# Kernel optimization log

Hardware: AMD Instinct MI355X
Metric: run time of the kernel (lower is better)

## Reference

```python
import jax, jax.numpy as jnp
import numpy as np

N = 50000   # nodes
E = 500000  # edges
G = 64      # graphs in batch
H = 2       # attention heads
D = 64      # hidden per head (hid)
F_IN = 4    # num_features
C = 5       # num_classes
NEG_SLOPE = 0.2


def setup_inputs() -> dict:
    key = jax.random.key(0)
    ks = jax.random.split(key, 24)
    inp = {
        'x': jax.random.normal(ks[0], (N, F_IN), jnp.float32),
        'edge_index': jax.random.randint(ks[1], (2, E), 0, N, dtype=jnp.int64),
        'batch': jnp.sort(jax.random.randint(ks[2], (N,), 0, G, dtype=jnp.int64)),
    }
    ins = [F_IN, H * D, H * D, H * D]
    ki = 3
    for l, fin in enumerate(ins, 1):
        s = 1.0 / np.sqrt(fin)
        inp[f'W{l}'] = s * jax.random.normal(ks[ki], (fin, H * D), jnp.float32); ki += 1
        inp[f'asrc{l}'] = 0.1 * jax.random.normal(ks[ki], (H, D), jnp.float32); ki += 1
        inp[f'adst{l}'] = 0.1 * jax.random.normal(ks[ki], (H, D), jnp.float32); ki += 1
        inp[f'b{l}'] = 0.01 * jax.random.normal(ks[ki], (H * D,), jnp.float32); ki += 1
    inp['lin_w'] = (1.0 / np.sqrt(H * D)) * jax.random.normal(ks[ki], (H * D, C), jnp.float32); ki += 1
    inp['lin_b'] = jnp.zeros((C,), jnp.float32)
    return inp


def gat_conv(x, src, dst, W, a_src, a_dst, b):
    # x: [N, Fin] -> h: [N, H, D]
    h = (x @ W).reshape(-1, H, D)
    alpha_src = jnp.sum(h * a_src, axis=-1)  # [N, H]
    alpha_dst = jnp.sum(h * a_dst, axis=-1)  # [N, H]
    e = jax.nn.leaky_relu(alpha_src[src] + alpha_dst[dst], NEG_SLOPE)  # [E, H]
    # segment softmax over incoming edges of each dst node
    e_max = jax.ops.segment_max(e, dst, num_segments=N)  # [N, H]
    e_exp = jnp.exp(e - e_max[dst])
    denom = jax.ops.segment_sum(e_exp, dst, num_segments=N)
    alpha = e_exp / (denom[dst] + 1e-16)  # [E, H]
    msg = h[src] * alpha[:, :, None]  # [E, H, D]
    out = jax.ops.segment_sum(msg, dst, num_segments=N)  # [N, H, D]
    return out.reshape(-1, H * D) + b


def reference(x, edge_index, batch,
              W1, asrc1, adst1, b1,
              W2, asrc2, adst2, b2,
              W3, asrc3, adst3, b3,
              W4, asrc4, adst4, b4,
              lin_w, lin_b):
    src, dst = edge_index[0], edge_index[1]
    h = jax.nn.relu(gat_conv(x, src, dst, W1, asrc1, adst1, b1))
    h = jax.nn.relu(gat_conv(h, src, dst, W2, asrc2, adst2, b2))
    h = jax.nn.relu(gat_conv(h, src, dst, W3, asrc3, adst3, b3))
    h = jax.nn.relu(gat_conv(h, src, dst, W4, asrc4, adst4, b4))
    # global mean pool over graphs
    sums = jax.ops.segment_sum(h, batch, num_segments=G)  # [G, 128]
    counts = jax.ops.segment_sum(jnp.ones((h.shape[0],), h.dtype), batch, num_segments=G)
    pooled = sums / jnp.maximum(counts, 1.0)[:, None]
    return jax.nn.sigmoid(pooled @ lin_w + lin_b)  # [G, C]
```

## Files before the change

kernel.cpp:

```cpp
#include <hip/hip_runtime.h>
#include <math.h>

#define NHEAD 2
#define NDIM  64
#define HD    128
#define NGRAPH 64
#define NCLS  5
#define NEG_SLOPE 0.2f
#define LDA 136

typedef __attribute__((ext_vector_type(8))) short bf16x8;
typedef __attribute__((ext_vector_type(4))) float f32x4;

static __device__ __forceinline__ unsigned short f2bf(float f) {
    unsigned int u = __float_as_uint(f);
    u = (u + 0x7fff + ((u >> 16) & 1)) >> 16;
    return (unsigned short)u;
}
static __device__ __forceinline__ float bf2f(unsigned short b) {
    return __uint_as_float((unsigned int)b << 16);
}


__global__ void k_deg(const int* __restrict__ dst, int* __restrict__ deg, int E) {
    int i = blockIdx.x * blockDim.x + threadIdx.x;
    if (i < E) atomicAdd(&deg[dst[i]], 1);
}

__global__ __launch_bounds__(256) void k_scan_local(const int* __restrict__ deg,
                                                    int* __restrict__ ptr,
                                                    int* __restrict__ bsum, int n) {
    __shared__ int wsum[4];
    const int tid = threadIdx.x, lane = tid & 63, wid = tid >> 6;
    const int base = blockIdx.x * 2048 + tid * 8;
    int v[8];
    #pragma unroll
    for (int k = 0; k < 8; ++k) {
        int i = base + k;
        v[k] = (i < n) ? deg[i] : 0;
    }
    #pragma unroll
    for (int k = 1; k < 8; ++k) v[k] += v[k - 1];
    int x = v[7];
    #pragma unroll
    for (int off = 1; off < 64; off <<= 1) {
        int t = __shfl_up(x, off, 64);
        if (lane >= off) x += t;
    }
    if (lane == 63) wsum[wid] = x;
    __syncthreads();
    int woff = 0;
    #pragma unroll
    for (int k = 0; k < 4; ++k) woff += (k < wid) ? wsum[k] : 0;
    int texcl = woff + x - v[7];
    #pragma unroll
    for (int k = 0; k < 8; ++k) {
        int i = base + k;
        if (i < n) ptr[i + 1] = texcl + v[k];
    }
    if (tid == 255) bsum[blockIdx.x] = woff + x;
    if (blockIdx.x == 0 && tid == 0) ptr[0] = 0;
}

__global__ void k_scan_bsum(int* __restrict__ bsum, int B) {
    int lane = threadIdx.x;
    int carry = 0;
    for (int base = 0; base < B; base += 64) {
        int i = base + lane;
        int v = (i < B) ? bsum[i] : 0;
        int x = v;
        #pragma unroll
        for (int off = 1; off < 64; off <<= 1) {
            int t = __shfl_up(x, off, 64);
            if (lane >= off) x += t;
        }
        if (i < B) bsum[i] = carry + x - v;
        carry += __shfl(x, 63, 64);
    }
}

__global__ __launch_bounds__(256) void k_scan_add(int* __restrict__ ptr,
                                                  const int* __restrict__ bsum, int n) {
    int off = bsum[blockIdx.x];
    if (off == 0) return;
    const int base = blockIdx.x * 2048 + threadIdx.x * 8;
    #pragma unroll
    for (int k = 0; k < 8; ++k) {
        int i = base + k;
        if (i < n) ptr[i + 1] += off;
    }
}

__global__ void k_scatter(const int* __restrict__ src, const int* __restrict__ dst,
                          const int* __restrict__ ptr, int* __restrict__ fill,
                          int* __restrict__ csr, int E) {
    int i = blockIdx.x * blockDim.x + threadIdx.x;
    if (i < E) {
        int d = dst[i];
        int pos = atomicAdd(&fill[d], 1);
        csr[ptr[d] + pos] = src[i];
    }
}


__global__ void k_prepw(const float* __restrict__ W2, const float* __restrict__ W3,
                        const float* __restrict__ W4, unsigned short* __restrict__ Wt) {
    int idx = blockIdx.x * blockDim.x + threadIdx.x;
    if (idx >= 3 * HD * HD) return;
    int l = idx / (HD * HD), rem = idx % (HD * HD);
    int n = rem >> 7, k = rem & 127;
    const float* W = (l == 0) ? W2 : (l == 1) ? W3 : W4;
    Wt[idx] = f2bf(W[k * HD + n]);
}

__global__ void k_gemm1_alpha(const float* __restrict__ x, const float* __restrict__ W,
                              const float* __restrict__ asrc, const float* __restrict__ adst,
                              unsigned short* __restrict__ out, float* __restrict__ oas,
                              float* __restrict__ oad, int N) {
    int n = (blockIdx.x * blockDim.x + threadIdx.x) >> 6;
    int lane = threadIdx.x & 63;
    if (n >= N) return;
    float4 xv = *(const float4*)&x[n * 4];
    int c0 = lane * 2;
    float2 w0 = *(const float2*)&W[c0];
    float2 w1 = *(const float2*)&W[128 + c0];
    float2 w2 = *(const float2*)&W[256 + c0];
    float2 w3 = *(const float2*)&W[384 + c0];
    float v0 = xv.x * w0.x + xv.y * w1.x + xv.z * w2.x + xv.w * w3.x;
    float v1 = xv.x * w0.y + xv.y * w1.y + xv.z * w2.y + xv.w * w3.y;
    unsigned short b0 = f2bf(v0), b1 = f2bf(v1);
    unsigned int packed = (unsigned int)b0 | ((unsigned int)b1 << 16);
    *(unsigned int*)&out[(size_t)n * HD + c0] = packed;
    float vx = bf2f(b0), vy = bf2f(b1);
    float2 av = *(const float2*)&asrc[c0];
    float2 dv = *(const float2*)&adst[c0];
    float s = vx * av.x + vy * av.y;
    float t = vx * dv.x + vy * dv.y;
    #pragma unroll
    for (int off = 16; off > 0; off >>= 1) {
        s += __shfl_xor(s, off);
        t += __shfl_xor(t, off);
    }
    if ((lane & 31) == 0) {
        int head = lane >> 5;
        oas[n * 2 + head] = s;
        oad[n * 2 + head] = t;
    }
}

static __device__ __forceinline__ uint4 agg_row(
    const unsigned short* __restrict__ h, const float* __restrict__ oas,
    const float* __restrict__ oad, const int* __restrict__ ptr,
    const int* __restrict__ csr, const float* __restrict__ bias,
    int n, int N, int sub, int gbase, int hsel) {
    const bool valid = (n < N);
    int beg = 0, end = 0;
    float2 adn = make_float2(0.f, 0.f);
    if (valid) {
        beg = ptr[n]; end = ptr[n + 1];
        adn = *(const float2*)&oad[n * 2];
    }
    float m0 = -INFINITY, m1 = -INFINITY, l0 = 0.f, l1 = 0.f;
    float acc[8];
    #pragma unroll
    for (int k = 0; k < 8; ++k) acc[k] = 0.f;

    auto accum = [&](uint4 hv, float pj) {
        #pragma unroll
        for (int k = 0; k < 4; ++k) {
            unsigned int u = (&hv.x)[k];
            acc[2 * k]     += pj * __uint_as_float(u << 16);
            acc[2 * k + 1] += pj * __uint_as_float(u & 0xffff0000u);
        }
    };

    int cbeg = beg;
    while (__any(cbeg < end)) {
        int rem = end - cbeg;
        int cnt = rem < 0 ? 0 : (rem > 16 ? 16 : rem);
        int s = 0;
        float e0 = -INFINITY, e1 = -INFINITY;
        if (sub < cnt) {
            s = csr[cbeg + sub];
            float2 as = *(const float2*)&oas[s * 2];
            e0 = as.x + adn.x; e0 = (e0 >= 0.f) ? e0 : NEG_SLOPE * e0;
            e1 = as.y + adn.y; e1 = (e1 >= 0.f) ? e1 : NEG_SLOPE * e1;
        }
        float c0 = e0, c1 = e1;
        #pragma unroll
        for (int off = 8; off > 0; off >>= 1) {
            c0 = fmaxf(c0, __shfl_xor(c0, off));
            c1 = fmaxf(c1, __shfl_xor(c1, off));
        }
        float nm0 = fmaxf(m0, c0), nm1 = fmaxf(m1, c1);
        float sc0 = (nm0 == -INFINITY) ? 0.f : __expf(m0 - nm0);
        float sc1 = (nm1 == -INFINITY) ? 0.f : __expf(m1 - nm1);
        float p0 = (sub < cnt) ? __expf(e0 - nm0) : 0.f;
        float p1 = (sub < cnt) ? __expf(e1 - nm1) : 0.f;
        float s0 = p0, s1 = p1;
        #pragma unroll
        for (int off = 8; off > 0; off >>= 1) {
            s0 += __shfl_xor(s0, off);
            s1 += __shfl_xor(s1, off);
        }
        l0 = l0 * sc0 + s0;
        l1 = l1 * sc1 + s1;
        m0 = nm0; m1 = nm1;
        float scl = hsel ? sc1 : sc0;
        #pragma unroll
        for (int k = 0; k < 8; ++k) acc[k] *= scl;

        int jm = cnt;
        jm = max(jm, __shfl_xor(jm, 16));
        jm = max(jm, __shfl_xor(jm, 32));

        auto fetchp = [&](int j, uint4& hv, float& pj) {
            int sj = __shfl(s, gbase + j);
            float pa = __shfl(p0, gbase + j);
            float pb = __shfl(p1, gbase + j);
            pj = hsel ? pb : pa;
            hv = make_uint4(0, 0, 0, 0);
            if (j < cnt)
                hv = *(const uint4*)&h[(size_t)sj * HD + sub * 8];
        };
        uint4 hA, hB = make_uint4(0, 0, 0, 0);
        float pA, pB = 0.f;
        fetchp(0, hA, pA);
        if (jm > 1) fetchp(1, hB, pB);
        for (int j = 2; j < jm; ++j) {
            uint4 hC; float pC;
            fetchp(j, hC, pC);
            accum(hA, pA);
            hA = hB; pA = pB;
            hB = hC; pB = pC;
        }
        accum(hA, pA);
        if (jm > 1) accum(hB, pB);

        cbeg += 16;
    }

    uint4 pk = make_uint4(0, 0, 0, 0);
    if (valid) {
        float lsel = hsel ? l1 : l0;
        float inv = 1.f / (lsel + 1e-16f);
        float4 ba = *(const float4*)&bias[sub * 8];
        float4 bb = *(const float4*)&bias[sub * 8 + 4];
        float o[8];
        o[0] = fmaxf(acc[0] * inv + ba.x, 0.f);
        o[1] = fmaxf(acc[1] * inv + ba.y, 0.f);
        o[2] = fmaxf(acc[2] * inv + ba.z, 0.f);
        o[3] = fmaxf(acc[3] * inv + ba.w, 0.f);
        o[4] = fmaxf(acc[4] * inv + bb.x, 0.f);
        o[5] = fmaxf(acc[5] * inv + bb.y, 0.f);
        o[6] = fmaxf(acc[6] * inv + bb.z, 0.f);
        o[7] = fmaxf(acc[7] * inv + bb.w, 0.f);
        pk.x = (unsigned int)f2bf(o[0]) | ((unsigned int)f2bf(o[1]) << 16);
        pk.y = (unsigned int)f2bf(o[2]) | ((unsigned int)f2bf(o[3]) << 16);
        pk.z = (unsigned int)f2bf(o[4]) | ((unsigned int)f2bf(o[5]) << 16);
        pk.w = (unsigned int)f2bf(o[6]) | ((unsigned int)f2bf(o[7]) << 16);
    }
    return pk;
}

__global__ __launch_bounds__(256, 8) void k_agg_gemm(
    const unsigned short* __restrict__ hin,
    const float* __restrict__ oas_in, const float* __restrict__ oad_in,
    const int* __restrict__ ptr, const int* __restrict__ csr,
    const float* __restrict__ bias,
    const unsigned short* __restrict__ Wt,
    const float* __restrict__ asrc, const float* __restrict__ adst,
    unsigned short* __restrict__ hout,
    float* __restrict__ oas_out, float* __restrict__ oad_out, int N) {
    __shared__ unsigned short As[16 * LDA];
    __shared__ float psL[4][16], pdL[4][16];
    const int tid = threadIdx.x;
    const int lane = tid & 63, w = tid >> 6;
    const int grp = lane >> 4, sub = lane & 15;
    const int gbase = lane & 48;
    const int hsel = sub >> 3;
    const int nbase = blockIdx.x * 16;

    const int row = w * 4 + grp;
    uint4 pk = agg_row(hin, oas_in, oad_in, ptr, csr, bias,
                       nbase + row, N, sub, gbase, hsel);
    *(uint4*)&As[(size_t)row * LDA + sub * 8] = pk;
    __syncthreads();

    float av2[2], dv2[2];
    #pragma unroll
    for (int i = 0; i < 2; ++i) {
        int c = w * 2 + i;
        av2[i] = asrc[c * 16 + sub];
        dv2[i] = adst[c * 16 + sub];
    }
    f32x4 acc[2];
    acc[0] = (f32x4)(0.f);
    acc[1] = (f32x4)(0.f);
    #pragma unroll
    for (int ks = 0; ks < 4; ++ks) {
        bf16x8 a0 = *(const bf16x8*)&As[(size_t)sub * LDA + ks * 32 + grp * 8];
        #pragma unroll
        for (int i = 0; i < 2; ++i) {
            int c = w * 2 + i;
            bf16x8 b = *(const bf16x8*)&Wt[(size_t)(c * 16 + sub) * HD + ks * 32 + grp * 8];
            acc[i] = __builtin_amdgcn_mfma_f32_16x16x32_bf16(a0, b, acc[i], 0, 0, 0);
        }
    }

    const int rowb = nbase + grp * 4;
    #pragma unroll
    for (int i = 0; i < 2; ++i) {
        int col = (w * 2 + i) * 16 + sub;
        #pragma unroll
        for (int r = 0; r < 4; ++r) {
            int rw = rowb + r;
            if (rw < N) hout[(size_t)rw * HD + col] = f2bf(acc[i][r]);
        }
    }
    #pragma unroll
    for (int r = 0; r < 4; ++r) {
        float ps = acc[0][r] * av2[0] + acc[1][r] * av2[1];
        float pd = acc[0][r] * dv2[0] + acc[1][r] * dv2[1];
        #pragma unroll
        for (int off = 1; off < 16; off <<= 1) {
            ps += __shfl_xor(ps, off);
            pd += __shfl_xor(pd, off);
        }
        if (sub == 0) {
            psL[w][grp * 4 + r] = ps;
            pdL[w][grp * 4 + r] = pd;
        }
    }
    __syncthreads();
    if (tid < 32) {
        int r2 = tid & 15, head = tid >> 4;
        int n2 = nbase + r2;
        if (n2 < N) {
            float s = psL[2 * head][r2] + psL[2 * head + 1][r2];
            float d = pdL[2 * head][r2] + pdL[2 * head + 1][r2];
            oas_out[n2 * 2 + head] = s;
            oad_out[n2 * 2 + head] = d;
        }
    }
}

__global__ __launch_bounds__(256) void k_agg_final(
    const unsigned short* __restrict__ hin,
    const float* __restrict__ oas_in, const float* __restrict__ oad_in,
    const int* __restrict__ ptr, const int* __restrict__ csr,
    const float* __restrict__ bias,
    unsigned short* __restrict__ out, int N) {
    const int tid = threadIdx.x;
    const int lane = tid & 63;
    const int grp = lane >> 4, sub = lane & 15;
    const int gbase = lane & 48;
    const int hsel = sub >> 3;
    const int n = ((blockIdx.x * blockDim.x + tid) >> 6) * 4 + grp;
    uint4 pk = agg_row(hin, oas_in, oad_in, ptr, csr, bias, n, N, sub, gbase, hsel);
    if (n < N) *(uint4*)&out[(size_t)n * HD + sub * 8] = pk;
}

__global__ void k_pool(const unsigned short* __restrict__ feat, const int* __restrict__ batch,
                       float* __restrict__ pooled, int* __restrict__ gcount, int N) {
    int col = threadIdx.x;
    int n0 = blockIdx.x * 128;
    int n1 = min(n0 + 128, N);
    float acc = 0.f;
    int curg = -1, runlen = 0;
    for (int n = n0; n < n1; ++n) {
        int g = batch[n];
        if (g != curg) {
            if (curg >= 0) {
                atomicAdd(&pooled[curg * HD + col], acc);
                if (col == 0) atomicAdd(&gcount[curg], runlen);
            }
            acc = 0.f; runlen = 0;
            curg = g;
        }
        acc += bf2f(feat[(size_t)n * HD + col]);
        runlen++;
    }
    if (curg >= 0) {
        atomicAdd(&pooled[curg * HD + col], acc);
        if (col == 0) atomicAdd(&gcount[curg], runlen);
    }
}

__global__ void k_final(const float* __restrict__ pooled, const int* __restrict__ gcount,
                        const float* __restrict__ lw, const float* __restrict__ lb,
                        float* __restrict__ out) {
    int tid = threadIdx.x;
    if (tid >= NGRAPH * NCLS) return;
    int g = tid / NCLS, c = tid % NCLS;
    float cnt = fmaxf((float)gcount[g], 1.f);
    const float* p = pooled + g * HD;
    float sum = 0.f;
    for (int k = 0; k < HD; ++k)
        sum += p[k] * lw[k * NCLS + c];
    float z = lb[c] + sum / cnt;
    out[tid] = 1.f / (1.f + __expf(-z));
}


static inline size_t al256(size_t x) { return (x + 255) & ~(size_t)255; }

extern "C" void kernel_launch(void* const* d_in, const int* in_sizes, int n_in,
                              void* d_out, int out_size, void* d_ws, size_t ws_size,
                              hipStream_t stream) {
    const int N = in_sizes[0] / 4;
    const int E = in_sizes[1] / 2;

    const float* x     = (const float*)d_in[0];
    const int*   esrc  = (const int*)d_in[1];
    const int*   edst  = esrc + E;
    const int*   batch = (const int*)d_in[2];
    const float* Wl[4]  = {(const float*)d_in[3],  (const float*)d_in[7],
                           (const float*)d_in[11], (const float*)d_in[15]};
    const float* asr[4] = {(const float*)d_in[4],  (const float*)d_in[8],
                           (const float*)d_in[12], (const float*)d_in[16]};
    const float* ads[4] = {(const float*)d_in[5],  (const float*)d_in[9],
                           (const float*)d_in[13], (const float*)d_in[17]};
    const float* bs[4]  = {(const float*)d_in[6],  (const float*)d_in[10],
                           (const float*)d_in[14], (const float*)d_in[18]};
    const float* lin_w = (const float*)d_in[19];
    const float* lin_b = (const float*)d_in[20];
    float* out = (float*)d_out;

    char* w = (char*)d_ws;
    size_t off = 0;
    auto alloc = [&](size_t bytes) -> void* {
        void* p = w + off;
        off = al256(off + bytes);
        return p;
    };
    int*   deg    = (int*)alloc((size_t)N * 4);
    int*   fill   = (int*)alloc((size_t)N * 4);
    int*   gcount = (int*)alloc((size_t)NGRAPH * 4);
    float* pooled = (float*)alloc((size_t)NGRAPH * HD * 4);
    size_t zbytes = off;
    int*   ptr    = (int*)alloc((size_t)(N + 1) * 4);
    int*   bsum   = (int*)alloc((size_t)1024 * 4);
    int*   csr    = (int*)alloc((size_t)E * 4);
    unsigned short* hA   = (unsigned short*)alloc((size_t)N * HD * 2);
    unsigned short* hB   = (unsigned short*)alloc((size_t)N * HD * 2);
    unsigned short* feat = (unsigned short*)alloc((size_t)N * HD * 2);
    unsigned short* Wt   = (unsigned short*)alloc((size_t)3 * HD * HD * 2);
    float* asA = (float*)alloc((size_t)N * 2 * 4);
    float* adA = (float*)alloc((size_t)N * 2 * 4);
    float* asB = (float*)alloc((size_t)N * 2 * 4);
    float* adB = (float*)alloc((size_t)N * 2 * 4);
    (void)ws_size; (void)n_in; (void)out_size;

    hipMemsetAsync(d_ws, 0, zbytes, stream);

    k_prepw<<<(3 * HD * HD + 255) / 256, 256, 0, stream>>>(Wl[1], Wl[2], Wl[3], Wt);
    k_deg<<<(E + 255) / 256, 256, 0, stream>>>(edst, deg, E);
    const int SB = (N + 2047) / 2048;
    k_scan_local<<<SB, 256, 0, stream>>>(deg, ptr, bsum, N);
    k_scan_bsum<<<1, 64, 0, stream>>>(bsum, SB);
    k_scan_add<<<SB, 256, 0, stream>>>(ptr, bsum, N);
    k_scatter<<<(E + 255) / 256, 256, 0, stream>>>(esrc, edst, ptr, fill, csr, E);

    const int fused_blocks = (N + 15) / 16;

    k_gemm1_alpha<<<(N + 3) / 4, 256, 0, stream>>>(
        x, Wl[0], asr[0], ads[0], hA, asA, adA, N);
    k_agg_gemm<<<fused_blocks, 256, 0, stream>>>(
        hA, asA, adA, ptr, csr, bs[0], Wt,
        asr[1], ads[1], hB, asB, adB, N);
    k_agg_gemm<<<fused_blocks, 256, 0, stream>>>(
        hB, asB, adB, ptr, csr, bs[1], Wt + (size_t)HD * HD,
        asr[2], ads[2], hA, asA, adA, N);
    k_agg_gemm<<<fused_blocks, 256, 0, stream>>>(
        hA, asA, adA, ptr, csr, bs[2], Wt + (size_t)2 * HD * HD,
        asr[3], ads[3], hB, asB, adB, N);
    k_agg_final<<<(N + 15) / 16, 256, 0, stream>>>(
        hB, asB, adB, ptr, csr, bs[3], feat, N);

    k_pool<<<(N + 127) / 128, 128, 0, stream>>>(feat, batch, pooled, gcount, N);
    k_final<<<1, 320, 0, stream>>>(pooled, gcount, lin_w, lin_b, out);
}
```

Before: 371.4 us.

## Precompute softmax denominators per node and drop online max in aggregation

Adds a pre-pass kernel per layer that computes each destination node's softmax denominator without max subtraction, clamping logits at 80 to avoid overflow. The aggregation then computes each edge weight directly as exp(e)*inv, with each lane walking the edges and issuing four gathers at a time, replacing the online-softmax rescaling, shuffles and cross-lane max and sum reductions. The fused GEMM output is also staged through shared memory so each row is written with coalesced 16-byte stores. The cost is an extra kernel launch and a second pass over the CSR edges per layer, plus a possible precision change from skipping max subtraction.

After: 357.5 us. -3.7%, faster.

```diff
diff --git a/kernel.cpp b/kernel.cpp
--- a/kernel.cpp
+++ b/kernel.cpp
@@ -148,124 +148,105 @@
     }
 }
 
-static __device__ __forceinline__ uint4 agg_row(
+__global__ __launch_bounds__(256) void k_node_inv(const int* __restrict__ ptr,
+                                                  const int* __restrict__ csr,
+                                                  const float* __restrict__ oas,
+                                                  const float* __restrict__ oad,
+                                                  float* __restrict__ invL, int N) {
+    int t = blockIdx.x * blockDim.x + threadIdx.x;
+    int n = t >> 2, l4 = t & 3;
+    if (n >= N) return;
+    int beg = ptr[n], end = ptr[n + 1];
+    float2 ad2 = *(const float2*)&oad[n * 2];
+    float s0 = 0.f, s1 = 0.f;
+    for (int j = beg + l4; j < end; j += 4) {
+        int s = csr[j];
+        float2 as2 = *(const float2*)&oas[s * 2];
+        float e0 = as2.x + ad2.x; e0 = (e0 >= 0.f) ? e0 : NEG_SLOPE * e0;
+        float e1 = as2.y + ad2.y; e1 = (e1 >= 0.f) ? e1 : NEG_SLOPE * e1;
+        e0 = fminf(e0, 80.f); e1 = fminf(e1, 80.f);
+        s0 += __expf(e0); s1 += __expf(e1);
+    }
+    s0 += __shfl_xor(s0, 1); s0 += __shfl_xor(s0, 2);
+    s1 += __shfl_xor(s1, 1); s1 += __shfl_xor(s1, 2);
+    if (l4 == 0)
+        *(float2*)&invL[n * 2] = make_float2(1.f / (s0 + 1e-16f), 1.f / (s1 + 1e-16f));
+}
+
+static __device__ __forceinline__ void agg_acc(
     const unsigned short* __restrict__ h, const float* __restrict__ oas,
-    const float* __restrict__ oad, const int* __restrict__ ptr,
-    const int* __restrict__ csr, const float* __restrict__ bias,
-    int n, int N, int sub, int gbase, int hsel) {
-    const bool valid = (n < N);
-    int beg = 0, end = 0;
-    float2 adn = make_float2(0.f, 0.f);
-    if (valid) {
-        beg = ptr[n]; end = ptr[n + 1];
-        adn = *(const float2*)&oad[n * 2];
-    }
-    float m0 = -INFINITY, m1 = -INFINITY, l0 = 0.f, l1 = 0.f;
-    float acc[8];
+    const float* __restrict__ oad, const float* __restrict__ invL,
+    const int* __restrict__ ptr, const int* __restrict__ csr,
+    int n, int N, int sub, int hsel, float* acc) {
     #pragma unroll
     for (int k = 0; k < 8; ++k) acc[k] = 0.f;
-
-    auto accum = [&](uint4 hv, float pj) {
+    if (n >= N) return;
+    const int beg = ptr[n], end = ptr[n + 1];
+    const float adh = oad[n * 2 + hsel];
+    const float inv = invL[n * 2 + hsel];
+
+    auto alpha = [&](float as) {
+        float e = as + adh;
+        e = (e >= 0.f) ? e : NEG_SLOPE * e;
+        e = fminf(e, 80.f);
+        return __expf(e) * inv;
+    };
+    auto accum = [&](uint4 hv, float a) {
         #pragma unroll
         for (int k = 0; k < 4; ++k) {
             unsigned int u = (&hv.x)[k];
-            acc[2 * k]     += pj * __uint_as_float(u << 16);
-            acc[2 * k + 1] += pj * __uint_as_float(u & 0xffff0000u);
+            acc[2 * k]     += a * __uint_as_float(u << 16);
+            acc[2 * k + 1] += a * __uint_as_float(u & 0xffff0000u);
         }
     };
 
-    int cbeg = beg;
-    while (__any(cbeg < end)) {
-        int rem = end - cbeg;
-        int cnt = rem < 0 ? 0 : (rem > 16 ? 16 : rem);
-        int s = 0;
-        float e0 = -INFINITY, e1 = -INFINITY;
-        if (sub < cnt) {
-            s = csr[cbeg + sub];
-            float2 as = *(const float2*)&oas[s * 2];
-            e0 = as.x + adn.x; e0 = (e0 >= 0.f) ? e0 : NEG_SLOPE * e0;
-            e1 = as.y + adn.y; e1 = (e1 >= 0.f) ? e1 : NEG_SLOPE * e1;
-        }
-        float c0 = e0, c1 = e1;
-        #pragma unroll
-        for (int off = 8; off > 0; off >>= 1) {
-            c0 = fmaxf(c0, __shfl_xor(c0, off));
-            c1 = fmaxf(c1, __shfl_xor(c1, off));
-        }
-        float nm0 = fmaxf(m0, c0), nm1 = fmaxf(m1, c1);
-        float sc0 = (nm0 == -INFINITY) ? 0.f : __expf(m0 - nm0);
-        float sc1 = (nm1 == -INFINITY) ? 0.f : __expf(m1 - nm1);
-        float p0 = (sub < cnt) ? __expf(e0 - nm0) : 0.f;
-        float p1 = (sub < cnt) ? __expf(e1 - nm1) : 0.f;
-        float s0 = p0, s1 = p1;
-        #pragma unroll
-        for (int off = 8; off > 0; off >>= 1) {
-            s0 += __shfl_xor(s0, off);
-            s1 += __shfl_xor(s1, off);
-        }
-        l0 = l0 * sc0 + s0;
-        l1 = l1 * sc1 + s1;
-        m0 = nm0; m1 = nm1;
-        float scl = hsel ? sc1 : sc0;
-        #pragma unroll
-        for (int k = 0; k < 8; ++k) acc[k] *= scl;
-
-        int jm = cnt;
-        jm = max(jm, __shfl_xor(jm, 16));
-        jm = max(jm, __shfl_xor(jm, 32));
-
-        auto fetchp = [&](int j, uint4& hv, float& pj) {
-            int sj = __shfl(s, gbase + j);
-            float pa = __shfl(p0, gbase + j);
-            float pb = __shfl(p1, gbase + j);
-            pj = hsel ? pb : pa;
-            hv = make_uint4(0, 0, 0, 0);
-            if (j < cnt)
-                hv = *(const uint4*)&h[(size_t)sj * HD + sub * 8];
-        };
-        uint4 hA, hB = make_uint4(0, 0, 0, 0);
-        float pA, pB = 0.f;
-        fetchp(0, hA, pA);
-        if (jm > 1) fetchp(1, hB, pB);
-        for (int j = 2; j < jm; ++j) {
-            uint4 hC; float pC;
-            fetchp(j, hC, pC);
-            accum(hA, pA);
-            hA = hB; pA = pB;
-            hB = hC; pB = pC;
-        }
-        accum(hA, pA);
-        if (jm > 1) accum(hB, pB);
-
-        cbeg += 16;
-    }
-
-    uint4 pk = make_uint4(0, 0, 0, 0);
-    if (valid) {
-        float lsel = hsel ? l1 : l0;
-        float inv = 1.f / (lsel + 1e-16f);
-        float4 ba = *(const float4*)&bias[sub * 8];
-        float4 bb = *(const float4*)&bias[sub * 8 + 4];
-        float o[8];
-        o[0] = fmaxf(acc[0] * inv + ba.x, 0.f);
-        o[1] = fmaxf(acc[1] * inv + ba.y, 0.f);
-        o[2] = fmaxf(acc[2] * inv + ba.z, 0.f);
-        o[3] = fmaxf(acc[3] * inv + ba.w, 0.f);
-        o[4] = fmaxf(acc[4] * inv + bb.x, 0.f);
-        o[5] = fmaxf(acc[5] * inv + bb.y, 0.f);
-        o[6] = fmaxf(acc[6] * inv + bb.z, 0.f);
-        o[7] = fmaxf(acc[7] * inv + bb.w, 0.f);
-        pk.x = (unsigned int)f2bf(o[0]) | ((unsigned int)f2bf(o[1]) << 16);
-        pk.y = (unsigned int)f2bf(o[2]) | ((unsigned int)f2bf(o[3]) << 16);
-        pk.z = (unsigned int)f2bf(o[4]) | ((unsigned int)f2bf(o[5]) << 16);
-        pk.w = (unsigned int)f2bf(o[6]) | ((unsigned int)f2bf(o[7]) << 16);
-    }
+    int j = beg;
+    for (; j + 4 <= end; j += 4) {
+        int s0 = csr[j], s1 = csr[j + 1], s2 = csr[j + 2], s3 = csr[j + 3];
+        uint4 h0 = *(const uint4*)&h[(size_t)s0 * HD + sub * 8];
+        uint4 h1 = *(const uint4*)&h[(size_t)s1 * HD + sub * 8];
+        uint4 h2 = *(const uint4*)&h[(size_t)s2 * HD + sub * 8];
+        uint4 h3 = *(const uint4*)&h[(size_t)s3 * HD + sub * 8];
+        float x0 = oas[s0 * 2 + hsel], x1 = oas[s1 * 2 + hsel];
+        float x2 = oas[s2 * 2 + hsel], x3 = oas[s3 * 2 + hsel];
+        accum(h0, alpha(x0));
+        accum(h1, alpha(x1));
+        accum(h2, alpha(x2));
+        accum(h3, alpha(x3));
+    }
+    for (; j < end; ++j) {
+        int s = csr[j];
+        uint4 hv = *(const uint4*)&h[(size_t)s * HD + sub * 8];
+        float xs = oas[s * 2 + hsel];
+        accum(hv, alpha(xs));
+    }
+}
+
+static __device__ __forceinline__ uint4 bias_relu_pack(
+    const float* acc, const float* __restrict__ bias, int sub) {
+    float4 ba = *(const float4*)&bias[sub * 8];
+    float4 bb = *(const float4*)&bias[sub * 8 + 4];
+    float o[8];
+    o[0] = fmaxf(acc[0] + ba.x, 0.f);
+    o[1] = fmaxf(acc[1] + ba.y, 0.f);
+    o[2] = fmaxf(acc[2] + ba.z, 0.f);
+    o[3] = fmaxf(acc[3] + ba.w, 0.f);
+    o[4] = fmaxf(acc[4] + bb.x, 0.f);
+    o[5] = fmaxf(acc[5] + bb.y, 0.f);
+    o[6] = fmaxf(acc[6] + bb.z, 0.f);
+    o[7] = fmaxf(acc[7] + bb.w, 0.f);
+    uint4 pk;
+    pk.x = (unsigned int)f2bf(o[0]) | ((unsigned int)f2bf(o[1]) << 16);
+    pk.y = (unsigned int)f2bf(o[2]) | ((unsigned int)f2bf(o[3]) << 16);
+    pk.z = (unsigned int)f2bf(o[4]) | ((unsigned int)f2bf(o[5]) << 16);
+    pk.w = (unsigned int)f2bf(o[6]) | ((unsigned int)f2bf(o[7]) << 16);
     return pk;
 }
 
 __global__ __launch_bounds__(256, 8) void k_agg_gemm(
     const unsigned short* __restrict__ hin,
     const float* __restrict__ oas_in, const float* __restrict__ oad_in,
+    const float* __restrict__ invL,
     const int* __restrict__ ptr, const int* __restrict__ csr,
     const float* __restrict__ bias,
     const unsigned short* __restrict__ Wt,
@@ -273,17 +254,18 @@
     unsigned short* __restrict__ hout,
     float* __restrict__ oas_out, float* __restrict__ oad_out, int N) {
     __shared__ unsigned short As[16 * LDA];
+    __shared__ unsigned short Ot[16][HD];
     __shared__ float psL[4][16], pdL[4][16];
     const int tid = threadIdx.x;
     const int lane = tid & 63, w = tid >> 6;
     const int grp = lane >> 4, sub = lane & 15;
-    const int gbase = lane & 48;
     const int hsel = sub >> 3;
     const int nbase = blockIdx.x * 16;
 
     const int row = w * 4 + grp;
-    uint4 pk = agg_row(hin, oas_in, oad_in, ptr, csr, bias,
-                       nbase + row, N, sub, gbase, hsel);
+    float acc8[8];
+    agg_acc(hin, oas_in, oad_in, invL, ptr, csr, nbase + row, N, sub, hsel, acc8);
+    uint4 pk = bias_relu_pack(acc8, bias, sub);
     *(uint4*)&As[(size_t)row * LDA + sub * 8] = pk;
     __syncthreads();
 
@@ -308,15 +290,12 @@
         }
     }
 
-    const int rowb = nbase + grp * 4;
     #pragma unroll
     for (int i = 0; i < 2; ++i) {
         int col = (w * 2 + i) * 16 + sub;
         #pragma unroll
-        for (int r = 0; r < 4; ++r) {
-            int rw = rowb + r;
-            if (rw < N) hout[(size_t)rw * HD + col] = f2bf(acc[i][r]);
-        }
+        for (int r = 0; r < 4; ++r)
+            Ot[grp * 4 + r][col] = f2bf(acc[i][r]);
     }
     #pragma unroll
     for (int r = 0; r < 4; ++r) {
@@ -333,6 +312,15 @@
         }
     }
     __syncthreads();
+
+    {
+        int r2 = tid >> 4, c16 = tid & 15;
+        int gn = nbase + r2;
+        if (gn < N) {
+            uint4 v = *(const uint4*)&Ot[r2][c16 * 8];
+            *(uint4*)&hout[(size_t)gn * HD + c16 * 8] = v;
+        }
+    }
     if (tid < 32) {
         int r2 = tid & 15, head = tid >> 4;
         int n2 = nbase + r2;
@@ -348,17 +336,21 @@
 __global__ __launch_bounds__(256) void k_agg_final(
     const unsigned short* __restrict__ hin,
     const float* __restrict__ oas_in, const float* __restrict__ oad_in,
+    const float* __restrict__ invL,
     const int* __restrict__ ptr, const int* __restrict__ csr,
     const float* __restrict__ bias,
     unsigned short* __restrict__ out, int N) {
     const int tid = threadIdx.x;
     const int lane = tid & 63;
     const int grp = lane >> 4, sub = lane & 15;
-    const int gbase = lane & 48;
     const int hsel = sub >> 3;
     const int n = ((blockIdx.x * blockDim.x + tid) >> 6) * 4 + grp;
-    uint4 pk = agg_row(hin, oas_in, oad_in, ptr, csr, bias, n, N, sub, gbase, hsel);
-    if (n < N) *(uint4*)&out[(size_t)n * HD + sub * 8] = pk;
+    float acc8[8];
+    agg_acc(hin, oas_in, oad_in, invL, ptr, csr, n, N, sub, hsel, acc8);
+    if (n < N) {
+        uint4 pk = bias_relu_pack(acc8, bias, sub);
+        *(uint4*)&out[(size_t)n * HD + sub * 8] = pk;
+    }
 }
 
 __global__ void k_pool(const unsigned short* __restrict__ feat, const int* __restrict__ batch,
@@ -442,6 +434,7 @@
     int*   ptr    = (int*)alloc((size_t)(N + 1) * 4);
     int*   bsum   = (int*)alloc((size_t)1024 * 4);
     int*   csr    = (int*)alloc((size_t)E * 4);
+    float* invL   = (float*)alloc((size_t)N * 2 * 4);
     unsigned short* hA   = (unsigned short*)alloc((size_t)N * HD * 2);
     unsigned short* hB   = (unsigned short*)alloc((size_t)N * HD * 2);
     unsigned short* feat = (unsigned short*)alloc((size_t)N * HD * 2);
@@ -462,21 +455,30 @@
     k_scan_add<<<SB, 256, 0, stream>>>(ptr, bsum, N);
     k_scatter<<<(E + 255) / 256, 256, 0, stream>>>(esrc, edst, ptr, fill, csr, E);
 
-    const int fused_blocks = (N + 15) / 16;
+    const int tblk = (N * 4 + 255) / 256;
+    const int fblk = (N + 15) / 16;
 
     k_gemm1_alpha<<<(N + 3) / 4, 256, 0, stream>>>(
         x, Wl[0], asr[0], ads[0], hA, asA, adA, N);
-    k_agg_gemm<<<fused_blocks, 256, 0, stream>>>(
-        hA, asA, adA, ptr, csr, bs[0], Wt,
-        asr[1], ads[1], hB, asB, adB, N);
-    k_agg_gemm<<<fused_blocks, 256, 0, stream>>>(
-        hB, asB, adB, ptr, csr, bs[1], Wt + (size_t)HD * HD,
-        asr[2], ads[2], hA, asA, adA, N);
-    k_agg_gemm<<<fused_blocks, 256, 0, stream>>>(
-        hA, asA, adA, ptr, csr, bs[2], Wt + (size_t)2 * HD * HD,
-        asr[3], ads[3], hB, asB, adB, N);
-    k_agg_final<<<(N + 15) / 16, 256, 0, stream>>>(
-        hB, asB, adB, ptr, csr, bs[3], feat, N);
+
+    const unsigned short* hc = hA; unsigned short* hn = hB;
+    const float* cas = asA; const float* cad = adA;
+    float* nas = asB;       float* nad = adB;
+    for (int i = 0; i < 4; ++i) {
+        k_node_inv<<<tblk, 256, 0, stream>>>(ptr, csr, cas, cad, invL, N);
+        if (i < 3) {
+            k_agg_gemm<<<fblk, 256, 0, stream>>>(
+                hc, cas, cad, invL, ptr, csr, bs[i],
+                Wt + (size_t)i * HD * HD, asr[i + 1], ads[i + 1],
+                hn, nas, nad, N);
+            const unsigned short* th = hc; hc = hn; hn = (unsigned short*)th;
+            const float* ts = cas; cas = nas; nas = (float*)ts;
+            const float* td = cad; cad = nad; nad = (float*)td;
+        } else {
+            k_agg_final<<<fblk, 256, 0, stream>>>(
+                hc, cas, cad, invL, ptr, csr, bs[i], feat, N);
+        }
+    }
 
     k_pool<<<(N + 127) / 128, 128, 0, stream>>>(feat, batch, pooled, gcount, N);
     k_final<<<1, 320, 0, stream>>>(pooled, gcount, lin_w, lin_b, out);
```
